# Performance work log

Measured on AMD Instinct MI355X. Metric: run time of the kernel, lower is better.

## Reference

```python
import jax, jax.numpy as jnp
import numpy as np

D = 512
B = 8
S1 = 2048
S2 = 2048


def _rope_cos_sin(seq_len, dim, dtype=jnp.float32):
    half = dim // 2
    inv_freq = 1.0 / (10000.0 ** (jnp.arange(half, dtype=jnp.float32) / half))
    t = jnp.arange(seq_len, dtype=jnp.float32)
    freqs = jnp.outer(t, inv_freq)                      # [S, D/2]
    emb = jnp.concatenate([freqs, freqs], axis=-1)      # [S, D]
    return jnp.cos(emb).astype(dtype), jnp.sin(emb).astype(dtype)


def _rotate_half(x):
    half = x.shape[-1] // 2
    return jnp.concatenate([-x[..., half:], x[..., :half]], axis=-1)


def _apply_rope(x, cos, sin):
    # x: [B, S, D]; cos/sin: [S, D]
    return x * cos[None, :, :] + _rotate_half(x) * sin[None, :, :]


def setup_inputs() -> dict:
    key = jax.random.key(0)
    ks = jax.random.split(key, 12)
    s = 1.0 / np.sqrt(D)
    return {
        "h1": jax.random.normal(ks[0], (B, S1, D), dtype=jnp.float32),
        "h2": jax.random.normal(ks[1], (B, S2, D), dtype=jnp.float32),
        "Wq": jax.random.normal(ks[2], (D, D), dtype=jnp.float32) * s,
        "bq": jnp.zeros((D,), dtype=jnp.float32),
        "Wk": jax.random.normal(ks[3], (D, D), dtype=jnp.float32) * s,
        "bk": jnp.zeros((D,), dtype=jnp.float32),
        "Wv": jax.random.normal(ks[4], (D, D), dtype=jnp.float32) * s,
        "bv": jnp.zeros((D,), dtype=jnp.float32),
        "Wo": jax.random.normal(ks[5], (D, D), dtype=jnp.float32) * s,
        "bo": jnp.zeros((D,), dtype=jnp.float32),
    }


def reference(h1, h2, Wq, bq, Wk, bk, Wv, bv, Wo, bo):
    d = h1.shape[-1]
    # Linear projections (torch Linear: x @ W.T + b)
    q = jnp.einsum("bsd,ed->bse", h1, Wq) + bq
    k = jnp.einsum("bsd,ed->bse", h2, Wk) + bk
    v = jnp.einsum("bsd,ed->bse", h2, Wv) + bv
    # RoPE on full hidden dim (single head)
    cos_q, sin_q = _rope_cos_sin(q.shape[1], d)
    cos_k, sin_k = _rope_cos_sin(k.shape[1], d)
    q = _apply_rope(q, cos_q, sin_q)
    k = _apply_rope(k, cos_k, sin_k)
    # scaled dot-product attention with full score matrix (faithful to source)
    energy = jnp.einsum("bqd,bkd->bqk", q, k) / jnp.sqrt(jnp.float32(d))
    attn = jax.nn.softmax(energy, axis=-1)
    out = jnp.einsum("bqk,bkd->bqd", attn, v)
    return jnp.einsum("bsd,ed->bse", out, Wo) + bo
```

## Files before the change

kernel.cpp:

```cpp
#include <hip/hip_runtime.h>
#include <stdint.h>

#define SCALE_E 0.044194173824159216f
#define LOG2_10000 13.287712379549449f
#define MCONST 8.0f

typedef __bf16 bf16x8 __attribute__((ext_vector_type(8)));
typedef float  f32x4  __attribute__((ext_vector_type(4)));

#define MFMA16(a, b, c) __builtin_amdgcn_mfma_f32_16x16x32_bf16((a), (b), (c), 0, 0, 0)

__device__ __forceinline__ void gload_lds16(const void* gp, void* lp) {
  __builtin_amdgcn_global_load_lds(
      reinterpret_cast<const uint32_t __attribute__((address_space(1)))*>(
          reinterpret_cast<uintptr_t>(gp)),
      reinterpret_cast<uint32_t __attribute__((address_space(3)))*>(
          reinterpret_cast<uintptr_t>(lp)),
      16, 0, 0);
}

__global__ __launch_bounds__(256) void gemm_split(
    const float* __restrict__ A, const float* __restrict__ W,
    const float* __restrict__ bias, float* __restrict__ C, int M)
{
  __shared__ __align__(16) __bf16 Als[2 * 512 * 8];
  __shared__ __align__(16) __bf16 Wls[2 * 512 * 8];

  const int t    = threadIdx.x;
  const int lane = t & 63;
  const int w    = t >> 6;
  const int m    = lane & 15;
  const int quad = lane >> 4;
  const int mw   = w & 1;
  const int nw   = w >> 1;
  const int m0   = blockIdx.y * 128;
  const int n0   = blockIdx.x * 128;

  const float* Ap0 = A + (size_t)(m0 + w * 16 + m) * 512 + quad * 8;
  const float* Ap1 = A + (size_t)(m0 + (w + 4) * 16 + m) * 512 + quad * 8;
  const float* Wp0 = W + (size_t)(n0 + w * 16 + m) * 512 + quad * 8;
  const float* Wp1 = W + (size_t)(n0 + (w + 4) * 16 + m) * 512 + quad * 8;

  f32x4 acc[4][4] = {};

  float4 ra[4], rw_[4];
  ra[0] = *(const float4*)(Ap0);     ra[1] = *(const float4*)(Ap0 + 4);
  ra[2] = *(const float4*)(Ap1);     ra[3] = *(const float4*)(Ap1 + 4);
  rw_[0] = *(const float4*)(Wp0);    rw_[1] = *(const float4*)(Wp0 + 4);
  rw_[2] = *(const float4*)(Wp1);    rw_[3] = *(const float4*)(Wp1 + 4);

  for (int kt = 0; kt < 512; kt += 32) {
    __syncthreads();
    #pragma unroll
    for (int h = 0; h < 2; ++h) {
      int slot = t + 256 * h;
      float v[8] = {ra[2*h].x, ra[2*h].y, ra[2*h].z, ra[2*h].w,
                    ra[2*h+1].x, ra[2*h+1].y, ra[2*h+1].z, ra[2*h+1].w};
      float u[8] = {rw_[2*h].x, rw_[2*h].y, rw_[2*h].z, rw_[2*h].w,
                    rw_[2*h+1].x, rw_[2*h+1].y, rw_[2*h+1].z, rw_[2*h+1].w};
      bf16x8 ah, al, bh, bl;
      #pragma unroll
      for (int j = 0; j < 8; ++j) {
        __bf16 hv = (__bf16)v[j];
        ah[j] = hv; al[j] = (__bf16)(v[j] - (float)hv);
        __bf16 hu = (__bf16)u[j];
        bh[j] = hu; bl[j] = (__bf16)(u[j] - (float)hu);
      }
      *(bf16x8*)&Als[(size_t)slot * 8]         = ah;
      *(bf16x8*)&Als[(size_t)(512 + slot) * 8] = al;
      *(bf16x8*)&Wls[(size_t)slot * 8]         = bh;
      *(bf16x8*)&Wls[(size_t)(512 + slot) * 8] = bl;
    }
    __syncthreads();

    if (kt + 32 < 512) {
      ra[0] = *(const float4*)(Ap0 + kt + 32);  ra[1] = *(const float4*)(Ap0 + kt + 36);
      ra[2] = *(const float4*)(Ap1 + kt + 32);  ra[3] = *(const float4*)(Ap1 + kt + 36);
      rw_[0] = *(const float4*)(Wp0 + kt + 32); rw_[1] = *(const float4*)(Wp0 + kt + 36);
      rw_[2] = *(const float4*)(Wp1 + kt + 32); rw_[3] = *(const float4*)(Wp1 + kt + 36);
    }

    bf16x8 ah[4], al[4], bh[4], bl[4];
    #pragma unroll
    for (int mt = 0; mt < 4; ++mt) {
      ah[mt] = *(const bf16x8*)&Als[(size_t)((mw * 4 + mt) * 64 + lane) * 8];
      al[mt] = *(const bf16x8*)&Als[(size_t)(512 + (mw * 4 + mt) * 64 + lane) * 8];
    }
    #pragma unroll
    for (int nt = 0; nt < 4; ++nt) {
      bh[nt] = *(const bf16x8*)&Wls[(size_t)((nw * 4 + nt) * 64 + lane) * 8];
      bl[nt] = *(const bf16x8*)&Wls[(size_t)(512 + (nw * 4 + nt) * 64 + lane) * 8];
    }
    #pragma unroll
    for (int mt = 0; mt < 4; ++mt)
      #pragma unroll
      for (int nt = 0; nt < 4; ++nt) {
        acc[mt][nt] = MFMA16(al[mt], bh[nt], acc[mt][nt]);
        acc[mt][nt] = MFMA16(ah[mt], bl[nt], acc[mt][nt]);
        acc[mt][nt] = MFMA16(ah[mt], bh[nt], acc[mt][nt]);
      }
  }

  float bv[4];
  #pragma unroll
  for (int nt = 0; nt < 4; ++nt) bv[nt] = bias[n0 + (nw * 4 + nt) * 16 + m];

  #pragma unroll
  for (int mt = 0; mt < 4; ++mt)
    #pragma unroll
    for (int r = 0; r < 4; ++r) {
      size_t row = m0 + (mw * 4 + mt) * 16 + quad * 4 + r;
      float* cp = C + row * 512 + n0;
      #pragma unroll
      for (int nt = 0; nt < 4; ++nt)
        cp[(nw * 4 + nt) * 16 + m] = acc[mt][nt][r] + bv[nt];
    }
}

__global__ __launch_bounds__(256) void rope_cast(
    const float* __restrict__ X, __bf16* __restrict__ Y, float scale)
{
  const int row = blockIdx.x;
  const int s = row & 2047;
  const int j = threadIdx.x;
  const float* p = X + (size_t)row * 512;
  __bf16* q = Y + (size_t)row * 512;
  float invf = exp2f((float)j * (-LOG2_10000 / 256.0f));
  float ang = (float)s * invf;
  float c = cosf(ang), sn = sinf(ang);
  float x1 = p[j], x2 = p[j + 256];
  q[j]       = (__bf16)((x1 * c - x2 * sn) * scale);
  q[j + 256] = (__bf16)((x2 * c + x1 * sn) * scale);
}

__global__ __launch_bounds__(256) void cast_transpose_v(
    const float* __restrict__ V, __bf16* __restrict__ Vt)
{
  __shared__ float tile[32][33];
  const int b  = blockIdx.z;
  const int s0 = blockIdx.x * 32;
  const int d0 = blockIdx.y * 32;
  const float* Vb = V + (size_t)b * 2048 * 512;
  __bf16* Vtb = Vt + (size_t)b * 512 * 2048;

  #pragma unroll
  for (int r = 0; r < 4; ++r) {
    int s = s0 + threadIdx.y + 8 * r;
    tile[threadIdx.y + 8 * r][threadIdx.x] = Vb[(size_t)s * 512 + d0 + threadIdx.x];
  }
  __syncthreads();
  #pragma unroll
  for (int r = 0; r < 4; ++r) {
    int d = d0 + threadIdx.y + 8 * r;
    Vtb[(size_t)d * 2048 + s0 + threadIdx.x] = (__bf16)tile[threadIdx.x][threadIdx.y + 8 * r];
  }
}

__global__ __launch_bounds__(512, 2) void attn_mfma(
    const __bf16* __restrict__ Qb, const __bf16* __restrict__ Kb,
    const __bf16* __restrict__ Vt, float* __restrict__ O)
{
  __shared__ __align__(16) __bf16 Kbuf[4096 * 8];
  __shared__ __align__(16) __bf16 Vbuf[4096 * 8];
  __shared__ __align__(16) __bf16 Ps[4096];
  __shared__ float l_sh[128];

  const int t    = threadIdx.x;
  const int b    = blockIdx.x >> 5;
  const int q0   = (blockIdx.x & 31) * 64;
  const int w    = t >> 6;
  const int lane = t & 63;
  const int m    = lane & 15;
  const int quad = lane >> 4;
  const int rw   = w >> 1;
  const int kp   = w & 1;

  const __bf16* Kbase = Kb + (size_t)b * 2048 * 512;
  const __bf16* Vbase = Vt + (size_t)b * 512 * 2048;

  const __bf16* qrow = Qb + ((size_t)b * 2048 + q0 + rw * 16 + m) * 512 + quad * 8;
  bf16x8 qf[16];
  #pragma unroll
  for (int kb = 0; kb < 16; ++kb) qf[kb] = *(const bf16x8*)(qrow + kb * 32);

  f32x4 o_acc[4][4] = {};
  float l_acc[4] = {};

  #pragma unroll
  for (int i = 0; i < 8; ++i) {
    const int j = w * 8 + i;
    gload_lds16(Kbase + (size_t)((j & 3) * 16 + m) * 512 + (j >> 2) * 32 + quad * 8,
                &Kbuf[(size_t)(j * 64 + lane) * 8]);
  }

  for (int kt = 0; kt < 2048; kt += 64) {
    __syncthreads();

    #pragma unroll
    for (int i = 0; i < 8; ++i) {
      const int j = w * 8 + i;
      gload_lds16(Vbase + (size_t)((j >> 1) * 16 + m) * 2048 + kt + (j & 1) * 32 + quad * 8,
                  &Vbuf[(size_t)(j * 64 + lane) * 8]);
    }

    f32x4 sc0 = {0.f, 0.f, 0.f, 0.f}, sc1 = {0.f, 0.f, 0.f, 0.f};
    #pragma unroll
    for (int kb = 0; kb < 16; ++kb) {
      bf16x8 k0 = *(const bf16x8*)&Kbuf[(size_t)((kb * 4 + kp * 2 + 0) * 64 + lane) * 8];
      bf16x8 k1 = *(const bf16x8*)&Kbuf[(size_t)((kb * 4 + kp * 2 + 1) * 64 + lane) * 8];
      sc0 = MFMA16(qf[kb], k0, sc0);
      sc1 = MFMA16(qf[kb], k1, sc1);
    }

    #pragma unroll
    for (int g = 0; g < 2; ++g) {
      const int kg = kp * 2 + g;
      f32x4 sc = g ? sc1 : sc0;
      float p0 = __expf(sc[0] - MCONST);
      float p1 = __expf(sc[1] - MCONST);
      float p2 = __expf(sc[2] - MCONST);
      float p3 = __expf(sc[3] - MCONST);
      {
        __bf16* pw = &Ps[(size_t)(((rw * 2 + (kg >> 1)) * 4 + ((kg & 1) * 2 + (m >> 3))) * 16
                                  + quad * 4) * 8 + (m & 7)];
        pw[0]  = (__bf16)p0;
        pw[8]  = (__bf16)p1;
        pw[16] = (__bf16)p2;
        pw[24] = (__bf16)p3;
      }
      float r0 = p0, r1 = p1, r2 = p2, r3 = p3;
      #pragma unroll
      for (int off = 1; off < 16; off <<= 1) {
        r0 += __shfl_xor(r0, off, 16);
        r1 += __shfl_xor(r1, off, 16);
        r2 += __shfl_xor(r2, off, 16);
        r3 += __shfl_xor(r3, off, 16);
      }
      l_acc[0] += r0; l_acc[1] += r1; l_acc[2] += r2; l_acc[3] += r3;
    }

    __syncthreads();

    if (kt + 64 < 2048) {
      #pragma unroll
      for (int i = 0; i < 8; ++i) {
        const int j = w * 8 + i;
        gload_lds16(Kbase + (size_t)(kt + 64 + (j & 3) * 16 + m) * 512 + (j >> 2) * 32 + quad * 8,
                    &Kbuf[(size_t)(j * 64 + lane) * 8]);
      }
    }

    #pragma unroll
    for (int kh = 0; kh < 2; ++kh) {
      bf16x8 pf[4];
      #pragma unroll
      for (int rg = 0; rg < 4; ++rg)
        pf[rg] = *(const bf16x8*)&Ps[(size_t)((rg * 2 + kh) * 64 + lane) * 8];
      #pragma unroll
      for (int dt = 0; dt < 4; ++dt) {
        bf16x8 vf = *(const bf16x8*)&Vbuf[(size_t)(((w * 4 + dt) * 2 + kh) * 64 + lane) * 8];
        o_acc[0][dt] = MFMA16(pf[0], vf, o_acc[0][dt]);
        o_acc[1][dt] = MFMA16(pf[1], vf, o_acc[1][dt]);
        o_acc[2][dt] = MFMA16(pf[2], vf, o_acc[2][dt]);
        o_acc[3][dt] = MFMA16(pf[3], vf, o_acc[3][dt]);
      }
    }
  }

  if (m == 0) {
    #pragma unroll
    for (int r = 0; r < 4; ++r)
      l_sh[kp * 64 + rw * 16 + quad * 4 + r] = l_acc[r];
  }
  __syncthreads();
  #pragma unroll
  for (int rt = 0; rt < 4; ++rt) {
    float invl[4];
    #pragma unroll
    for (int r = 0; r < 4; ++r)
      invl[r] = 1.0f / (l_sh[rt * 16 + quad * 4 + r] + l_sh[64 + rt * 16 + quad * 4 + r]);
    #pragma unroll
    for (int dt = 0; dt < 4; ++dt)
      #pragma unroll
      for (int r = 0; r < 4; ++r) {
        size_t row = (size_t)b * 2048 + q0 + rt * 16 + quad * 4 + r;
        O[row * 512 + w * 64 + dt * 16 + m] = o_acc[rt][dt][r] * invl[r];
      }
  }
}

extern "C" void kernel_launch(void* const* d_in, const int* in_sizes, int n_in,
                              void* d_out, int out_size, void* d_ws, size_t ws_size,
                              hipStream_t stream)
{
  const float* h1 = (const float*)d_in[0];
  const float* h2 = (const float*)d_in[1];
  const float* Wq = (const float*)d_in[2];
  const float* bq = (const float*)d_in[3];
  const float* Wk = (const float*)d_in[4];
  const float* bk = (const float*)d_in[5];
  const float* Wv = (const float*)d_in[6];
  const float* bv = (const float*)d_in[7];
  const float* Wo = (const float*)d_in[8];
  const float* bo = (const float*)d_in[9];
  float* out = (float*)d_out;

  const size_t MB = 1024 * 1024;

  float*  Qf  = (float*)d_ws;
  float*  Kf  = (float*)((char*)d_ws + 32 * MB);
  float*  O2  = (float*)((char*)d_ws + 16 * MB);
  __bf16* Vtb = (__bf16*)d_ws;
  __bf16* Qbb = (__bf16*)((char*)d_ws + 64 * MB);
  __bf16* Kbb = (__bf16*)((char*)d_ws + 80 * MB);
  float*  Vf  = out;

  const int M = 8 * 2048;
  dim3 gG(4, M / 128);

  gemm_split<<<gG, 256, 0, stream>>>(h1, Wq, bq, Qf, M);
  gemm_split<<<gG, 256, 0, stream>>>(h2, Wk, bk, Kf, M);
  gemm_split<<<gG, 256, 0, stream>>>(h2, Wv, bv, Vf, M);
  rope_cast<<<M, 256, 0, stream>>>(Qf, Qbb, SCALE_E);
  rope_cast<<<M, 256, 0, stream>>>(Kf, Kbb, 1.0f);
  cast_transpose_v<<<dim3(64, 16, 8), dim3(32, 8), 0, stream>>>(Vf, Vtb);
  attn_mfma<<<256, 512, 0, stream>>>(Qbb, Kbb, Vtb, O2);
  gemm_split<<<gG, 256, 0, stream>>>(O2, Wo, bo, out, M);
}
```

Baseline: 415.1 us.

## Remap QK waves to share K fragments and compute row sums via MFMA

Each wave now handles two 16-row query tiles against one 16-key column group, so every K fragment read from LDS feeds two MFMAs instead of one and the Q register footprint doubles. The softmax row-sum is no longer built with per-row shuffle reductions; it is computed by an extra MFMA of the P tile against a ones vector during the PV phase. s_setprio hints are added around the MFMA sections. In exchange, register pressure rises from the doubled Q fragments, and the row sum is now taken over the bf16-rounded P values.

```diff
diff --git a/kernel.cpp b/kernel.cpp
--- a/kernel.cpp
+++ b/kernel.cpp
@@ -172,19 +172,29 @@
   const int lane = t & 63;
   const int m    = lane & 15;
   const int quad = lane >> 4;
-  const int rw   = w >> 1;
-  const int kp   = w & 1;
+  const int rw2  = w >> 2;
+  const int kp   = w & 3;
+  const int lrg  = w >> 1;
+  const int lkh  = w & 1;
 
   const __bf16* Kbase = Kb + (size_t)b * 2048 * 512;
   const __bf16* Vbase = Vt + (size_t)b * 512 * 2048;
 
-  const __bf16* qrow = Qb + ((size_t)b * 2048 + q0 + rw * 16 + m) * 512 + quad * 8;
-  bf16x8 qf[16];
-  #pragma unroll
-  for (int kb = 0; kb < 16; ++kb) qf[kb] = *(const bf16x8*)(qrow + kb * 32);
+  const __bf16* qlo = Qb + ((size_t)b * 2048 + q0 + rw2 * 16 + m) * 512 + quad * 8;
+  const __bf16* qhi = qlo + (size_t)32 * 512;
+  bf16x8 qfl[16], qfh[16];
+  #pragma unroll
+  for (int kb = 0; kb < 16; ++kb) {
+    qfl[kb] = *(const bf16x8*)(qlo + kb * 32);
+    qfh[kb] = *(const bf16x8*)(qhi + kb * 32);
+  }
+
+  bf16x8 onesf;
+  #pragma unroll
+  for (int j = 0; j < 8; ++j) onesf[j] = (__bf16)1.0f;
 
   f32x4 o_acc[4][4] = {};
-  float l_acc[4] = {};
+  f32x4 l_tile = {0.f, 0.f, 0.f, 0.f};
 
   #pragma unroll
   for (int i = 0; i < 8; ++i) {
@@ -204,39 +214,29 @@
     }
 
     f32x4 sc0 = {0.f, 0.f, 0.f, 0.f}, sc1 = {0.f, 0.f, 0.f, 0.f};
+    __builtin_amdgcn_s_setprio(1);
     #pragma unroll
     for (int kb = 0; kb < 16; ++kb) {
-      bf16x8 k0 = *(const bf16x8*)&Kbuf[(size_t)((kb * 4 + kp * 2 + 0) * 64 + lane) * 8];
-      bf16x8 k1 = *(const bf16x8*)&Kbuf[(size_t)((kb * 4 + kp * 2 + 1) * 64 + lane) * 8];
-      sc0 = MFMA16(qf[kb], k0, sc0);
-      sc1 = MFMA16(qf[kb], k1, sc1);
-    }
+      bf16x8 kf = *(const bf16x8*)&Kbuf[(size_t)((kb * 4 + kp) * 64 + lane) * 8];
+      sc0 = MFMA16(qfl[kb], kf, sc0);
+      sc1 = MFMA16(qfh[kb], kf, sc1);
+    }
+    __builtin_amdgcn_s_setprio(0);
 
     #pragma unroll
     for (int g = 0; g < 2; ++g) {
-      const int kg = kp * 2 + g;
+      const int rg = rw2 + 2 * g;
       f32x4 sc = g ? sc1 : sc0;
       float p0 = __expf(sc[0] - MCONST);
       float p1 = __expf(sc[1] - MCONST);
       float p2 = __expf(sc[2] - MCONST);
       float p3 = __expf(sc[3] - MCONST);
-      {
-        __bf16* pw = &Ps[(size_t)(((rw * 2 + (kg >> 1)) * 4 + ((kg & 1) * 2 + (m >> 3))) * 16
-                                  + quad * 4) * 8 + (m & 7)];
-        pw[0]  = (__bf16)p0;
-        pw[8]  = (__bf16)p1;
-        pw[16] = (__bf16)p2;
-        pw[24] = (__bf16)p3;
-      }
-      float r0 = p0, r1 = p1, r2 = p2, r3 = p3;
-      #pragma unroll
-      for (int off = 1; off < 16; off <<= 1) {
-        r0 += __shfl_xor(r0, off, 16);
-        r1 += __shfl_xor(r1, off, 16);
-        r2 += __shfl_xor(r2, off, 16);
-        r3 += __shfl_xor(r3, off, 16);
-      }
-      l_acc[0] += r0; l_acc[1] += r1; l_acc[2] += r2; l_acc[3] += r3;
+      __bf16* pw = &Ps[(size_t)(((rg * 2 + (kp >> 1)) * 4 + ((kp & 1) * 2 + (m >> 3))) * 16
+                                + quad * 4) * 8 + (m & 7)];
+      pw[0]  = (__bf16)p0;
+      pw[8]  = (__bf16)p1;
+      pw[16] = (__bf16)p2;
+      pw[24] = (__bf16)p3;
     }
 
     __syncthreads();
@@ -250,12 +250,15 @@
       }
     }
 
+    __builtin_amdgcn_s_setprio(1);
     #pragma unroll
     for (int kh = 0; kh < 2; ++kh) {
       bf16x8 pf[4];
       #pragma unroll
       for (int rg = 0; rg < 4; ++rg)
         pf[rg] = *(const bf16x8*)&Ps[(size_t)((rg * 2 + kh) * 64 + lane) * 8];
+      if (kh == lkh)
+        l_tile = MFMA16(pf[lrg], onesf, l_tile);
       #pragma unroll
       for (int dt = 0; dt < 4; ++dt) {
         bf16x8 vf = *(const bf16x8*)&Vbuf[(size_t)(((w * 4 + dt) * 2 + kh) * 64 + lane) * 8];
@@ -265,12 +268,13 @@
         o_acc[3][dt] = MFMA16(pf[3], vf, o_acc[3][dt]);
       }
     }
+    __builtin_amdgcn_s_setprio(0);
   }
 
   if (m == 0) {
     #pragma unroll
     for (int r = 0; r < 4; ++r)
-      l_sh[kp * 64 + rw * 16 + quad * 4 + r] = l_acc[r];
+      l_sh[lkh * 64 + lrg * 16 + quad * 4 + r] = l_tile[r];
   }
   __syncthreads();
   #pragma unroll
```

Result: slower. 548.4 us (+32.1%).

## Load V directly to registers, compute row sums via MFMA, reorder blocks by batch

Applied to the files above, without the earlier changes.

V tiles are no longer staged through LDS; each wave loads its own V fragments from global memory straight into registers, which frees the Vbuf shared allocation. The softmax denominator is now computed by an MFMA of P against a ones vector instead of shuffle reductions. The block-to-batch mapping is interleaved so concurrent blocks cover different batches, and s_setprio raises wave priority around the MFMA sections. The costs are more VGPR pressure and uncoalesced or exposed global V load latency in exchange for less LDS traffic and fewer shuffles.

```diff
diff --git a/kernel.cpp b/kernel.cpp
--- a/kernel.cpp
+++ b/kernel.cpp
@@ -161,13 +161,12 @@
     const __bf16* __restrict__ Vt, float* __restrict__ O)
 {
   __shared__ __align__(16) __bf16 Kbuf[4096 * 8];
-  __shared__ __align__(16) __bf16 Vbuf[4096 * 8];
   __shared__ __align__(16) __bf16 Ps[4096];
   __shared__ float l_sh[128];
 
   const int t    = threadIdx.x;
-  const int b    = blockIdx.x >> 5;
-  const int q0   = (blockIdx.x & 31) * 64;
+  const int b    = blockIdx.x & 7;
+  const int q0   = (blockIdx.x >> 3) * 64;
   const int w    = t >> 6;
   const int lane = t & 63;
   const int m    = lane & 15;
@@ -183,8 +182,14 @@
   #pragma unroll
   for (int kb = 0; kb < 16; ++kb) qf[kb] = *(const bf16x8*)(qrow + kb * 32);
 
+  bf16x8 onesf;
+  #pragma unroll
+  for (int j = 0; j < 8; ++j) onesf[j] = (__bf16)1.0f;
+
   f32x4 o_acc[4][4] = {};
-  float l_acc[4] = {};
+  f32x4 l_tile = {0.f, 0.f, 0.f, 0.f};
+
+  const __bf16* vrow = Vbase + (size_t)(w * 64 + m) * 2048;
 
   #pragma unroll
   for (int i = 0; i < 8; ++i) {
@@ -196,14 +201,16 @@
   for (int kt = 0; kt < 2048; kt += 64) {
     __syncthreads();
 
-    #pragma unroll
-    for (int i = 0; i < 8; ++i) {
-      const int j = w * 8 + i;
-      gload_lds16(Vbase + (size_t)((j >> 1) * 16 + m) * 2048 + kt + (j & 1) * 32 + quad * 8,
-                  &Vbuf[(size_t)(j * 64 + lane) * 8]);
-    }
+    bf16x8 vf[8];
+    #pragma unroll
+    for (int dt = 0; dt < 4; ++dt)
+      #pragma unroll
+      for (int kh = 0; kh < 2; ++kh)
+        vf[dt * 2 + kh] =
+            *(const bf16x8*)(vrow + (size_t)dt * 16 * 2048 + kt + kh * 32 + quad * 8);
 
     f32x4 sc0 = {0.f, 0.f, 0.f, 0.f}, sc1 = {0.f, 0.f, 0.f, 0.f};
+    __builtin_amdgcn_s_setprio(1);
     #pragma unroll
     for (int kb = 0; kb < 16; ++kb) {
       bf16x8 k0 = *(const bf16x8*)&Kbuf[(size_t)((kb * 4 + kp * 2 + 0) * 64 + lane) * 8];
@@ -211,6 +218,7 @@
       sc0 = MFMA16(qf[kb], k0, sc0);
       sc1 = MFMA16(qf[kb], k1, sc1);
     }
+    __builtin_amdgcn_s_setprio(0);
 
     #pragma unroll
     for (int g = 0; g < 2; ++g) {
@@ -220,23 +228,12 @@
       float p1 = __expf(sc[1] - MCONST);
       float p2 = __expf(sc[2] - MCONST);
       float p3 = __expf(sc[3] - MCONST);
-      {
-        __bf16* pw = &Ps[(size_t)(((rw * 2 + (kg >> 1)) * 4 + ((kg & 1) * 2 + (m >> 3))) * 16
-                                  + quad * 4) * 8 + (m & 7)];
-        pw[0]  = (__bf16)p0;
-        pw[8]  = (__bf16)p1;
-        pw[16] = (__bf16)p2;
-        pw[24] = (__bf16)p3;
-      }
-      float r0 = p0, r1 = p1, r2 = p2, r3 = p3;
-      #pragma unroll
-      for (int off = 1; off < 16; off <<= 1) {
-        r0 += __shfl_xor(r0, off, 16);
-        r1 += __shfl_xor(r1, off, 16);
-        r2 += __shfl_xor(r2, off, 16);
-        r3 += __shfl_xor(r3, off, 16);
-      }
-      l_acc[0] += r0; l_acc[1] += r1; l_acc[2] += r2; l_acc[3] += r3;
+      __bf16* pw = &Ps[(size_t)(((rw * 2 + (kg >> 1)) * 4 + ((kg & 1) * 2 + (m >> 3))) * 16
+                                + quad * 4) * 8 + (m & 7)];
+      pw[0]  = (__bf16)p0;
+      pw[8]  = (__bf16)p1;
+      pw[16] = (__bf16)p2;
+      pw[24] = (__bf16)p3;
     }
 
     __syncthreads();
@@ -250,27 +247,31 @@
       }
     }
 
+    __builtin_amdgcn_s_setprio(1);
     #pragma unroll
     for (int kh = 0; kh < 2; ++kh) {
       bf16x8 pf[4];
       #pragma unroll
       for (int rg = 0; rg < 4; ++rg)
         pf[rg] = *(const bf16x8*)&Ps[(size_t)((rg * 2 + kh) * 64 + lane) * 8];
+      if (kh == kp)
+        l_tile = MFMA16(pf[rw], onesf, l_tile);
       #pragma unroll
       for (int dt = 0; dt < 4; ++dt) {
-        bf16x8 vf = *(const bf16x8*)&Vbuf[(size_t)(((w * 4 + dt) * 2 + kh) * 64 + lane) * 8];
-        o_acc[0][dt] = MFMA16(pf[0], vf, o_acc[0][dt]);
-        o_acc[1][dt] = MFMA16(pf[1], vf, o_acc[1][dt]);
-        o_acc[2][dt] = MFMA16(pf[2], vf, o_acc[2][dt]);
-        o_acc[3][dt] = MFMA16(pf[3], vf, o_acc[3][dt]);
-      }
-    }
+        bf16x8 vv = vf[dt * 2 + kh];
+        o_acc[0][dt] = MFMA16(pf[0], vv, o_acc[0][dt]);
+        o_acc[1][dt] = MFMA16(pf[1], vv, o_acc[1][dt]);
+        o_acc[2][dt] = MFMA16(pf[2], vv, o_acc[2][dt]);
+        o_acc[3][dt] = MFMA16(pf[3], vv, o_acc[3][dt]);
+      }
+    }
+    __builtin_amdgcn_s_setprio(0);
   }
 
   if (m == 0) {
     #pragma unroll
     for (int r = 0; r < 4; ++r)
-      l_sh[kp * 64 + rw * 16 + quad * 4 + r] = l_acc[r];
+      l_sh[kp * 64 + rw * 16 + quad * 4 + r] = l_tile[r];
   }
   __syncthreads();
   #pragma unroll
```

New measurement: 472.7 us. 1.14x slower.
